# Kernel tuning notes

Measured on AMD Instinct MI355X. Metric: run time of the kernel, lower is better.

The kernel has to match this reference:

```python
import jax, jax.numpy as jnp
import numpy as np

N = 20000      # nodes
E = 200000     # edges
F_IN = 512     # num_features
H = 1024       # hidden (hard-coded in module)
OUT = 128      # output_size


def setup_inputs() -> dict:
    key = jax.random.key(0)
    ks = jax.random.split(key, 12)
    x = jax.random.normal(ks[0], (N, F_IN), jnp.float32)
    edge_index = jax.random.randint(ks[1], (2, E), 0, N, dtype=jnp.int32)
    edge_weight = jax.random.uniform(ks[2], (E,), jnp.float32)
    # GCNConv weights (glorot-ish) and biases
    w1 = jax.random.normal(ks[3], (F_IN, H), jnp.float32) / np.sqrt(F_IN)
    b1 = jnp.zeros((H,), jnp.float32)
    w2 = jax.random.normal(ks[4], (H, OUT), jnp.float32) / np.sqrt(H)
    b2 = jnp.zeros((OUT,), jnp.float32)
    # residual Linear layers
    rw1 = jax.random.normal(ks[5], (F_IN, H), jnp.float32) / np.sqrt(F_IN)
    rb1 = jax.random.normal(ks[6], (H,), jnp.float32) * 0.01
    rw2 = jax.random.normal(ks[7], (H, OUT), jnp.float32) / np.sqrt(H)
    rb2 = jax.random.normal(ks[8], (OUT,), jnp.float32) * 0.01
    return {"x": x, "w1": w1, "b1": b1, "w2": w2, "b2": b2,
            "rw1": rw1, "rb1": rb1, "rw2": rw2, "rb2": rb2,
            "edge_weight": edge_weight, "edge_index": edge_index}


def gcn_conv(x, W, b, edge_index, edge_weight, n):
    """PyG GCNConv: linear transform, add self-loops (weight 1), sym-normalized scatter-add."""
    xw = x @ W                                             # [n, d_out]
    loop = jnp.arange(n, dtype=edge_index.dtype)
    row = jnp.concatenate([edge_index[0], loop])           # sources (x_j)
    col = jnp.concatenate([edge_index[1], loop])           # targets (aggregate here)
    ew = jnp.concatenate([edge_weight, jnp.ones((n,), xw.dtype)])
    deg = jax.ops.segment_sum(ew, col, num_segments=n)     # weighted in-degree
    dis = jnp.where(deg > 0, jax.lax.rsqrt(jnp.where(deg > 0, deg, 1.0)), 0.0)
    norm = dis[row] * ew * dis[col]                        # [E+n]
    msg = xw[row] * norm[:, None]                          # gather + scale
    out = jax.ops.segment_sum(msg, col, num_segments=n)    # scatter-add
    return out + b


def reference(x, w1, b1, w2, b2, rw1, rb1, rw2, rb2, edge_weight, edge_index):
    n = x.shape[0]
    h = jax.nn.relu(gcn_conv(x, w1, b1, edge_index, edge_weight, n) + (x @ rw1 + rb1))
    # F.dropout(training=False) is identity in eval mode
    out = gcn_conv(h, w2, b2, edge_index, edge_weight, n) + (h @ rw2 + rb2)
    return out
```

## Files before the change

### kernel.cpp

```cpp
#include <hip/hip_runtime.h>
#include <hip/hip_bf16.h>

#define NN 20000
#define EE 200000
#define FIN 512
#define HID 1024
#define OUTF 128
#define MPAD 20096

typedef unsigned short ush;
typedef __attribute__((ext_vector_type(8))) short bf16x8;
typedef __attribute__((ext_vector_type(4))) float f32x4;

__device__ __forceinline__ ush f2bf_rne(float f) {
    union { float f; unsigned u; } a; a.f = f;
    unsigned u = a.u;
    return (ush)((u + 0x7fffu + ((u >> 16) & 1u)) >> 16);
}
__device__ __forceinline__ float bf2f(ush h) {
    union { float f; unsigned u; } a; a.u = ((unsigned)h) << 16;
    return a.f;
}
__device__ __forceinline__ void split_bf(float v, ush& hi, ush& lo) {
    hi = f2bf_rne(v);
    lo = f2bf_rne(v - bf2f(hi));
}

__device__ __forceinline__ void gl16(const void* g, void* l) {
    __builtin_amdgcn_global_load_lds(
        (const __attribute__((address_space(1))) unsigned*)g,
        (__attribute__((address_space(3))) unsigned*)l, 16, 0, 0);
}

__global__ void init_kernel(float* deg, int* cnt, int n) {
    int i = blockIdx.x * blockDim.x + threadIdx.x;
    if (i < n) { deg[i] = 1.0f; cnt[i] = 0; }
}

__global__ void deg_count_kernel(const int* __restrict__ ei, const float* __restrict__ ew,
                                 float* deg, int* cnt, int e) {
    int idx = blockIdx.x * blockDim.x + threadIdx.x;
    if (idx < e) {
        int c = ei[EE + idx];
        atomicAdd(&deg[c], ew[idx]);
        atomicAdd(&cnt[c], 1);
    }
}

__global__ void dis_kernel(const float* __restrict__ deg, float* dis, int n) {
    int i = blockIdx.x * blockDim.x + threadIdx.x;
    if (i < n) dis[i] = rsqrtf(deg[i]);
}

__global__ void bias_kernel(const float* __restrict__ b1, const float* __restrict__ rb1,
                            const float* __restrict__ b2, const float* __restrict__ rb2,
                            float* bias1s, float* bias2c) {
    int i = blockIdx.x * blockDim.x + threadIdx.x;
    if (i < HID) bias1s[i] = b1[i] + rb1[i];
    if (i < 256) bias2c[i] = (i < 128) ? 0.0f : (b2[i - 128] + rb2[i - 128]);
}

#define SCAN_THREADS 1024
#define SCAN_CHUNK 20
__global__ __launch_bounds__(SCAN_THREADS)
void scan_kernel(const int* __restrict__ cnt, int* rowptr, int* cursor, int n, int total_e) {
    __shared__ int part[SCAN_THREADS];
    int t = threadIdx.x;
    int base = t * SCAN_CHUNK;
    int s = 0;
    for (int j = 0; j < SCAN_CHUNK; ++j) { int i = base + j; if (i < n) s += cnt[i]; }
    part[t] = s;
    __syncthreads();
    for (int off = 1; off < SCAN_THREADS; off <<= 1) {
        int add = (t >= off) ? part[t - off] : 0;
        __syncthreads();
        part[t] += add;
        __syncthreads();
    }
    int run = (t == 0) ? 0 : part[t - 1];
    for (int j = 0; j < SCAN_CHUNK; ++j) {
        int i = base + j;
        if (i < n) { rowptr[i] = run; cursor[i] = run; run += cnt[i]; }
    }
    if (t == SCAN_THREADS - 1) rowptr[n] = total_e;
}

__global__ void scatter_kernel(const int* __restrict__ ei, const float* __restrict__ ew,
                               const float* __restrict__ dis, int* cursor,
                               int* srcs, float* norms, int e) {
    int idx = blockIdx.x * blockDim.x + threadIdx.x;
    if (idx < e) {
        int r = ei[idx];
        int c = ei[EE + idx];
        float nv = dis[r] * ew[idx] * dis[c];
        int p = atomicAdd(&cursor[c], 1);
        srcs[p] = r;
        norms[p] = nv;
    }
}

__global__ __launch_bounds__(256)
void tsplit_kernel(const float* __restrict__ src, int K, int N,
                   ush* __restrict__ dh, ush* __restrict__ dl, int ldst, int koff) {
    __shared__ float tile[32][33];
    int tx = threadIdx.x & 31, ty = threadIdx.x >> 5;
    int n0 = blockIdx.x * 32, k0 = blockIdx.y * 32;
#pragma unroll
    for (int i = 0; i < 4; ++i)
        tile[ty * 4 + i][tx] = src[(size_t)(k0 + ty * 4 + i) * N + n0 + tx];
    __syncthreads();
#pragma unroll
    for (int i = 0; i < 4; ++i) {
        int n = n0 + ty * 4 + i, k = k0 + tx;
        float v = tile[tx][ty * 4 + i];
        ush h, lo; split_bf(v, h, lo);
        size_t off = (size_t)n * ldst + koff + k;
        dh[off] = h;
        dl[off] = lo;
    }
}

__global__ __launch_bounds__(128)
void aggx_kernel(const float* __restrict__ x,
                 ush* __restrict__ xh, ush* __restrict__ xl,
                 ush* __restrict__ axh, ush* __restrict__ axl,
                 const float* __restrict__ dis,
                 const int* __restrict__ rowptr, const int* __restrict__ srcs,
                 const float* __restrict__ norms) {
    int i = blockIdx.x;
    int t = threadIdx.x;
    float d = dis[i];
    float d2 = d * d;
    float4 v = ((const float4*)(x + (size_t)i * FIN))[t];

    ushort4 vh, vl;
    split_bf(v.x, vh.x, vl.x); split_bf(v.y, vh.y, vl.y);
    split_bf(v.z, vh.z, vl.z); split_bf(v.w, vh.w, vl.w);
    ((ushort4*)(xh + (size_t)i * FIN))[t] = vh;
    ((ushort4*)(xl + (size_t)i * FIN))[t] = vl;

    float s0 = d2 * v.x, s1 = d2 * v.y, s2 = d2 * v.z, s3 = d2 * v.w;
    int beg = rowptr[i], end = rowptr[i + 1];
    int j = beg;
    for (; j + 2 <= end; j += 2) {
        int sa = srcs[j], sb = srcs[j + 1];
        float wa = norms[j], wb = norms[j + 1];
        float4 ua = ((const float4*)(x + (size_t)sa * FIN))[t];
        float4 ub = ((const float4*)(x + (size_t)sb * FIN))[t];
        s0 += wa * ua.x + wb * ub.x;
        s1 += wa * ua.y + wb * ub.y;
        s2 += wa * ua.z + wb * ub.z;
        s3 += wa * ua.w + wb * ub.w;
    }
    if (j < end) {
        int sa = srcs[j];
        float wa = norms[j];
        float4 ua = ((const float4*)(x + (size_t)sa * FIN))[t];
        s0 += wa * ua.x; s1 += wa * ua.y; s2 += wa * ua.z; s3 += wa * ua.w;
    }
    ushort4 hv, lv;
    split_bf(s0, hv.x, lv.x); split_bf(s1, hv.y, lv.y);
    split_bf(s2, hv.z, lv.z); split_bf(s3, hv.w, lv.w);
    ((ushort4*)(axh + (size_t)i * FIN))[t] = hv;
    ((ushort4*)(axl + (size_t)i * FIN))[t] = lv;
}

__global__ __launch_bounds__(256)
void gemm_mfma(const ush* __restrict__ A0h, const ush* __restrict__ A0l,
               const ush* __restrict__ A1h, const ush* __restrict__ A1l,
               int ksw, int KA,
               const ush* __restrict__ BTh, const ush* __restrict__ BTl,
               const float* __restrict__ bias,
               float* __restrict__ Cf, ush* __restrict__ Chh, ush* __restrict__ Chl,
               int M, int N, int K, int mode) {
    __shared__ ush Ah[128 * 32], Al[128 * 32], Bh[128 * 32], Bl[128 * 32];

    int t = threadIdx.x;
    int l = t & 63, w = t >> 6;
    int wr = w >> 1, wc = w & 1;
    int bm = blockIdx.y * 128, bn = blockIdx.x * 128;

    int sr = t >> 2;
    int sg8 = (t & 3) * 8;
    size_t a_off0 = (size_t)(bm + sr) * KA + sg8;
    size_t a_off1 = (size_t)(bm + 64 + sr) * KA + sg8;
    size_t b_off0 = (size_t)(bn + sr) * K + sg8;
    size_t b_off1 = (size_t)(bn + 64 + sr) * K + sg8;
    int lo0 = t * 16, lo1 = t * 16 + 4096;

    int abase = (wr * 64 + (l & 15)) * 64 + ((l >> 4) << 4);
    int bbase = (wc * 64 + (l & 15)) * 64 + ((l >> 4) << 4);

    f32x4 acc[4][4];
#pragma unroll
    for (int i = 0; i < 4; ++i)
#pragma unroll
        for (int j = 0; j < 4; ++j) acc[i][j] = (f32x4){0.f, 0.f, 0.f, 0.f};

    for (int kt = 0; kt < K; kt += 32) {
        const ush* Asrch; const ush* Asrcl; int kk;
        if (kt < ksw) { Asrch = A0h; Asrcl = A0l; kk = kt; }
        else          { Asrch = A1h; Asrcl = A1l; kk = kt - ksw; }

        gl16(Asrch + a_off0 + kk, (char*)Ah + lo0);
        gl16(Asrch + a_off1 + kk, (char*)Ah + lo1);
        gl16(Asrcl + a_off0 + kk, (char*)Al + lo0);
        gl16(Asrcl + a_off1 + kk, (char*)Al + lo1);
        gl16(BTh + b_off0 + kt, (char*)Bh + lo0);
        gl16(BTh + b_off1 + kt, (char*)Bh + lo1);
        gl16(BTl + b_off0 + kt, (char*)Bl + lo0);
        gl16(BTl + b_off1 + kt, (char*)Bl + lo1);
        __syncthreads();

        bf16x8 ah[4], al[4], bh[4], bl[4];
#pragma unroll
        for (int f = 0; f < 4; ++f) {
            ah[f] = *(const bf16x8*)((const char*)Ah + abase + f * 1024);
            al[f] = *(const bf16x8*)((const char*)Al + abase + f * 1024);
            bh[f] = *(const bf16x8*)((const char*)Bh + bbase + f * 1024);
            bl[f] = *(const bf16x8*)((const char*)Bl + bbase + f * 1024);
        }
#pragma unroll
        for (int fm = 0; fm < 4; ++fm)
#pragma unroll
            for (int fn = 0; fn < 4; ++fn)
                acc[fm][fn] = __builtin_amdgcn_mfma_f32_16x16x32_bf16(ah[fm], bh[fn], acc[fm][fn], 0, 0, 0);
#pragma unroll
        for (int fm = 0; fm < 4; ++fm)
#pragma unroll
            for (int fn = 0; fn < 4; ++fn)
                acc[fm][fn] = __builtin_amdgcn_mfma_f32_16x16x32_bf16(ah[fm], bl[fn], acc[fm][fn], 0, 0, 0);
#pragma unroll
        for (int fm = 0; fm < 4; ++fm)
#pragma unroll
            for (int fn = 0; fn < 4; ++fn)
                acc[fm][fn] = __builtin_amdgcn_mfma_f32_16x16x32_bf16(al[fm], bh[fn], acc[fm][fn], 0, 0, 0);
        __syncthreads();
    }

    int ccol = bn + wc * 64 + (l & 15);
    float bb[4];
#pragma unroll
    for (int fn = 0; fn < 4; ++fn) bb[fn] = bias ? bias[ccol + fn * 16] : 0.0f;

    if (mode) {
#pragma unroll
        for (int fm = 0; fm < 4; ++fm)
#pragma unroll
            for (int j = 0; j < 4; ++j) {
                int row = bm + wr * 64 + fm * 16 + ((l >> 4) << 2) + j;
                if (row < M) {
#pragma unroll
                    for (int fn = 0; fn < 4; ++fn) {
                        float v = fmaxf(acc[fm][fn][j] + bb[fn], 0.0f);
                        ush hi, lo; split_bf(v, hi, lo);
                        size_t off = (size_t)row * N + ccol + fn * 16;
                        Chh[off] = hi;
                        Chl[off] = lo;
                    }
                }
            }
    } else {
#pragma unroll
        for (int fm = 0; fm < 4; ++fm)
#pragma unroll
            for (int j = 0; j < 4; ++j) {
                int row = bm + wr * 64 + fm * 16 + ((l >> 4) << 2) + j;
                if (row < M) {
#pragma unroll
                    for (int fn = 0; fn < 4; ++fn)
                        Cf[(size_t)row * N + ccol + fn * 16] = acc[fm][fn][j] + bb[fn];
                }
            }
    }
}

__global__ __launch_bounds__(256)
void agg2_kernel(const float* __restrict__ z2, const float* __restrict__ dis,
                 const int* __restrict__ rowptr, const int* __restrict__ srcs,
                 const float* __restrict__ norms, float* __restrict__ out) {
    int wave = threadIdx.x >> 6;
    int lane = threadIdx.x & 63;
    int i = blockIdx.x * 4 + wave;
    float d = dis[i];
    float d2 = d * d;
    float2 v = ((const float2*)(z2 + (size_t)i * 256))[lane];
    float ax = d2 * v.x, ay = d2 * v.y;
    int beg = rowptr[i], end = rowptr[i + 1];
    int j = beg;
    for (; j + 2 <= end; j += 2) {
        int sa = srcs[j], sb = srcs[j + 1];
        float wa = norms[j], wb = norms[j + 1];
        float2 ua = ((const float2*)(z2 + (size_t)sa * 256))[lane];
        float2 ub = ((const float2*)(z2 + (size_t)sb * 256))[lane];
        ax += wa * ua.x + wb * ub.x;
        ay += wa * ua.y + wb * ub.y;
    }
    if (j < end) {
        int sa = srcs[j];
        float wa = norms[j];
        float2 ua = ((const float2*)(z2 + (size_t)sa * 256))[lane];
        ax += wa * ua.x; ay += wa * ua.y;
    }
    float2 r = ((const float2*)(z2 + (size_t)i * 256 + 128))[lane];
    float2 o; o.x = ax + r.x; o.y = ay + r.y;
    ((float2*)(out + (size_t)i * OUTF))[lane] = o;
}

extern "C" void kernel_launch(void* const* d_in, const int* in_sizes, int n_in,
                              void* d_out, int out_size, void* d_ws, size_t ws_size,
                              hipStream_t stream) {
    const float* x   = (const float*)d_in[0];
    const float* w1  = (const float*)d_in[1];
    const float* b1  = (const float*)d_in[2];
    const float* w2  = (const float*)d_in[3];
    const float* b2  = (const float*)d_in[4];
    const float* rw1 = (const float*)d_in[5];
    const float* rb1 = (const float*)d_in[6];
    const float* rw2 = (const float*)d_in[7];
    const float* rb2 = (const float*)d_in[8];
    const float* ew  = (const float*)d_in[9];
    const int*   ei  = (const int*)d_in[10];
    float* out = (float*)d_out;

    char* p = (char*)d_ws;
    ush* xh  = (ush*)p; p += (size_t)MPAD * FIN * 2;
    ush* xl  = (ush*)p; p += (size_t)MPAD * FIN * 2;
    ush* axh = (ush*)p; p += (size_t)MPAD * FIN * 2;
    ush* axl = (ush*)p; p += (size_t)MPAD * FIN * 2;
    ush* hh  = (ush*)p; p += (size_t)MPAD * HID * 2;
    ush* hl  = (ush*)p; p += (size_t)MPAD * HID * 2;
    ush* w1cth = (ush*)p; p += (size_t)HID * HID * 2;
    ush* w1ctl = (ush*)p; p += (size_t)HID * HID * 2;
    ush* w2cth = (ush*)p; p += (size_t)256 * HID * 2;
    ush* w2ctl = (ush*)p; p += (size_t)256 * HID * 2;
    float* deg    = (float*)p; p += NN * 4;
    float* dis    = (float*)p; p += NN * 4;
    float* norms  = (float*)p; p += EE * 4;
    float* bias1s = (float*)p; p += HID * 4;
    float* bias2c = (float*)p; p += 256 * 4;
    int* rowptr = (int*)p; p += (NN + 1) * 4;
    int* cursor = (int*)p; p += NN * 4;
    int* cnt    = (int*)p; p += NN * 4;
    int* srcs   = (int*)p; p += EE * 4;
    float* z2 = (float*)xh;

    init_kernel<<<(NN + 255) / 256, 256, 0, stream>>>(deg, cnt, NN);
    deg_count_kernel<<<(EE + 255) / 256, 256, 0, stream>>>(ei, ew, deg, cnt, EE);
    dis_kernel<<<(NN + 255) / 256, 256, 0, stream>>>(deg, dis, NN);
    bias_kernel<<<(HID + 255) / 256, 256, 0, stream>>>(b1, rb1, b2, rb2, bias1s, bias2c);
    scan_kernel<<<1, SCAN_THREADS, 0, stream>>>(cnt, rowptr, cursor, NN, EE);
    scatter_kernel<<<(EE + 255) / 256, 256, 0, stream>>>(ei, ew, dis, cursor, srcs, norms, EE);

    { dim3 g(HID / 32, FIN / 32); tsplit_kernel<<<g, 256, 0, stream>>>(w1,  FIN, HID, w1cth, w1ctl, HID, 0);   }
    { dim3 g(HID / 32, FIN / 32); tsplit_kernel<<<g, 256, 0, stream>>>(rw1, FIN, HID, w1cth, w1ctl, HID, FIN); }
    { dim3 g(OUTF / 32, HID / 32); tsplit_kernel<<<g, 256, 0, stream>>>(w2,  HID, OUTF, w2cth, w2ctl, HID, 0); }
    { dim3 g(OUTF / 32, HID / 32); tsplit_kernel<<<g, 256, 0, stream>>>(rw2, HID, OUTF,
                                        w2cth + (size_t)128 * HID, w2ctl + (size_t)128 * HID, HID, 0); }

    aggx_kernel<<<NN, 128, 0, stream>>>(x, xh, xl, axh, axl, dis, rowptr, srcs, norms);

    {
        dim3 grid(HID / 128, MPAD / 128);
        gemm_mfma<<<grid, 256, 0, stream>>>(axh, axl, xh, xl, FIN, FIN,
                                            w1cth, w1ctl, bias1s,
                                            nullptr, hh, hl,
                                            NN, HID, HID, 1);
    }
    {
        dim3 grid(256 / 128, MPAD / 128);
        gemm_mfma<<<grid, 256, 0, stream>>>(hh, hl, hh, hl, HID, HID,
                                            w2cth, w2ctl, bias2c,
                                            z2, nullptr, nullptr,
                                            NN, 256, HID, 0);
    }
    agg2_kernel<<<NN / 4, 256, 0, stream>>>(z2, dis, rowptr, srcs, norms, out);
}
```

Before: 467.9 us.

## Double-buffer LDS tiles in MFMA GEMM and remap workgroups across XCDs

```diff
diff --git a/kernel.cpp b/kernel.cpp
--- a/kernel.cpp
+++ b/kernel.cpp
@@ -173,12 +173,19 @@
                const float* __restrict__ bias,
                float* __restrict__ Cf, ush* __restrict__ Chh, ush* __restrict__ Chl,
                int M, int N, int K, int mode) {
-    __shared__ ush Ah[128 * 32], Al[128 * 32], Bh[128 * 32], Bl[128 * 32];
+    __shared__ ush Ah[2][128 * 32], Al[2][128 * 32], Bh[2][128 * 32], Bl[2][128 * 32];
+
+    int nwg = gridDim.x * gridDim.y;
+    int orig = blockIdx.y * gridDim.x + blockIdx.x;
+    int xcd = orig & 7, slot = orig >> 3;
+    int q = nwg >> 3, r = nwg & 7;
+    int wg = (xcd < r ? xcd * (q + 1) : r * (q + 1) + (xcd - r) * q) + slot;
+    int bn = (wg % gridDim.x) * 128;
+    int bm = (wg / gridDim.x) * 128;
 
     int t = threadIdx.x;
     int l = t & 63, w = t >> 6;
     int wr = w >> 1, wc = w & 1;
-    int bm = blockIdx.y * 128, bn = blockIdx.x * 128;
 
     int sr = t >> 2;
     int sg8 = (t & 3) * 8;
@@ -191,34 +198,40 @@
     int abase = (wr * 64 + (l & 15)) * 64 + ((l >> 4) << 4);
     int bbase = (wc * 64 + (l & 15)) * 64 + ((l >> 4) << 4);
 
-    f32x4 acc[4][4];
-#pragma unroll
-    for (int i = 0; i < 4; ++i)
-#pragma unroll
-        for (int j = 0; j < 4; ++j) acc[i][j] = (f32x4){0.f, 0.f, 0.f, 0.f};
-
-    for (int kt = 0; kt < K; kt += 32) {
+    auto stage = [&](int kt, int b) {
         const ush* Asrch; const ush* Asrcl; int kk;
         if (kt < ksw) { Asrch = A0h; Asrcl = A0l; kk = kt; }
         else          { Asrch = A1h; Asrcl = A1l; kk = kt - ksw; }
-
-        gl16(Asrch + a_off0 + kk, (char*)Ah + lo0);
-        gl16(Asrch + a_off1 + kk, (char*)Ah + lo1);
-        gl16(Asrcl + a_off0 + kk, (char*)Al + lo0);
-        gl16(Asrcl + a_off1 + kk, (char*)Al + lo1);
-        gl16(BTh + b_off0 + kt, (char*)Bh + lo0);
-        gl16(BTh + b_off1 + kt, (char*)Bh + lo1);
-        gl16(BTl + b_off0 + kt, (char*)Bl + lo0);
-        gl16(BTl + b_off1 + kt, (char*)Bl + lo1);
-        __syncthreads();
+        gl16(Asrch + a_off0 + kk, (char*)Ah[b] + lo0);
+        gl16(Asrch + a_off1 + kk, (char*)Ah[b] + lo1);
+        gl16(Asrcl + a_off0 + kk, (char*)Al[b] + lo0);
+        gl16(Asrcl + a_off1 + kk, (char*)Al[b] + lo1);
+        gl16(BTh + b_off0 + kt, (char*)Bh[b] + lo0);
+        gl16(BTh + b_off1 + kt, (char*)Bh[b] + lo1);
+        gl16(BTl + b_off0 + kt, (char*)Bl[b] + lo0);
+        gl16(BTl + b_off1 + kt, (char*)Bl[b] + lo1);
+    };
+
+    f32x4 acc[4][4];
+#pragma unroll
+    for (int i = 0; i < 4; ++i)
+#pragma unroll
+        for (int j = 0; j < 4; ++j) acc[i][j] = (f32x4){0.f, 0.f, 0.f, 0.f};
+
+    stage(0, 0);
+    __syncthreads();
+
+    int cur = 0;
+    for (int kt = 0; kt < K; kt += 32) {
+        if (kt + 32 < K) stage(kt + 32, cur ^ 1);
 
         bf16x8 ah[4], al[4], bh[4], bl[4];
 #pragma unroll
         for (int f = 0; f < 4; ++f) {
-            ah[f] = *(const bf16x8*)((const char*)Ah + abase + f * 1024);
-            al[f] = *(const bf16x8*)((const char*)Al + abase + f * 1024);
-            bh[f] = *(const bf16x8*)((const char*)Bh + bbase + f * 1024);
-            bl[f] = *(const bf16x8*)((const char*)Bl + bbase + f * 1024);
+            ah[f] = *(const bf16x8*)((const char*)Ah[cur] + abase + f * 1024);
+            al[f] = *(const bf16x8*)((const char*)Al[cur] + abase + f * 1024);
+            bh[f] = *(const bf16x8*)((const char*)Bh[cur] + bbase + f * 1024);
+            bl[f] = *(const bf16x8*)((const char*)Bl[cur] + bbase + f * 1024);
         }
 #pragma unroll
         for (int fm = 0; fm < 4; ++fm)
@@ -235,7 +248,9 @@
 #pragma unroll
             for (int fn = 0; fn < 4; ++fn)
                 acc[fm][fn] = __builtin_amdgcn_mfma_f32_16x16x32_bf16(al[fm], bh[fn], acc[fm][fn], 0, 0, 0);
+
         __syncthreads();
+        cur ^= 1;
     }
 
     int ccol = bn + wc * 64 + (l & 15);
```

New measurement: 465.2 us. No clear change (-0.6%).

## Remap GEMM workgroups per XCD and fold small setup kernels together

Applied to the files above, without the earlier changes.

```diff
diff --git a/kernel.cpp b/kernel.cpp
--- a/kernel.cpp
+++ b/kernel.cpp
@@ -6,7 +6,7 @@
 #define FIN 512
 #define HID 1024
 #define OUTF 128
-#define MPAD 20096
+#define MPAD 20224
 
 typedef unsigned short ush;
 typedef __attribute__((ext_vector_type(8))) short bf16x8;
@@ -32,9 +32,14 @@
         (__attribute__((address_space(3))) unsigned*)l, 16, 0, 0);
 }
 
-__global__ void init_kernel(float* deg, int* cnt, int n) {
+__global__ void init_kernel(float* deg, int* cnt, int n,
+                            const float* __restrict__ b1, const float* __restrict__ rb1,
+                            const float* __restrict__ b2, const float* __restrict__ rb2,
+                            float* bias1s, float* bias2c) {
     int i = blockIdx.x * blockDim.x + threadIdx.x;
     if (i < n) { deg[i] = 1.0f; cnt[i] = 0; }
+    if (i < HID) bias1s[i] = b1[i] + rb1[i];
+    if (i < 256) bias2c[i] = (i < 128) ? 0.0f : (b2[i - 128] + rb2[i - 128]);
 }
 
 __global__ void deg_count_kernel(const int* __restrict__ ei, const float* __restrict__ ew,
@@ -47,28 +52,19 @@
     }
 }
 
-__global__ void dis_kernel(const float* __restrict__ deg, float* dis, int n) {
-    int i = blockIdx.x * blockDim.x + threadIdx.x;
-    if (i < n) dis[i] = rsqrtf(deg[i]);
-}
-
-__global__ void bias_kernel(const float* __restrict__ b1, const float* __restrict__ rb1,
-                            const float* __restrict__ b2, const float* __restrict__ rb2,
-                            float* bias1s, float* bias2c) {
-    int i = blockIdx.x * blockDim.x + threadIdx.x;
-    if (i < HID) bias1s[i] = b1[i] + rb1[i];
-    if (i < 256) bias2c[i] = (i < 128) ? 0.0f : (b2[i - 128] + rb2[i - 128]);
-}
-
 #define SCAN_THREADS 1024
 #define SCAN_CHUNK 20
 __global__ __launch_bounds__(SCAN_THREADS)
-void scan_kernel(const int* __restrict__ cnt, int* rowptr, int* cursor, int n, int total_e) {
+void scan_kernel(const int* __restrict__ cnt, int* rowptr, int* cursor, int n, int total_e,
+                 const float* __restrict__ deg, float* __restrict__ dis) {
     __shared__ int part[SCAN_THREADS];
     int t = threadIdx.x;
     int base = t * SCAN_CHUNK;
     int s = 0;
-    for (int j = 0; j < SCAN_CHUNK; ++j) { int i = base + j; if (i < n) s += cnt[i]; }
+    for (int j = 0; j < SCAN_CHUNK; ++j) {
+        int i = base + j;
+        if (i < n) { s += cnt[i]; dis[i] = rsqrtf(deg[i]); }
+    }
     part[t] = s;
     __syncthreads();
     for (int off = 1; off < SCAN_THREADS; off <<= 1) {
@@ -175,10 +171,17 @@
                int M, int N, int K, int mode) {
     __shared__ ush Ah[128 * 32], Al[128 * 32], Bh[128 * 32], Bl[128 * 32];
 
+    int nwg = gridDim.x * gridDim.y;
+    int orig = blockIdx.y * gridDim.x + blockIdx.x;
+    int xcd = orig & 7, slot = orig >> 3;
+    int q = nwg >> 3, r = nwg & 7;
+    int wg = (xcd < r ? xcd * (q + 1) : r * (q + 1) + (xcd - r) * q) + slot;
+    int bn = (wg % gridDim.x) * 128;
+    int bm = (wg / gridDim.x) * 128;
+
     int t = threadIdx.x;
     int l = t & 63, w = t >> 6;
     int wr = w >> 1, wc = w & 1;
-    int bm = blockIdx.y * 128, bn = blockIdx.x * 128;
 
     int sr = t >> 2;
     int sg8 = (t & 3) * 8;
@@ -302,8 +305,8 @@
         float2 ua = ((const float2*)(z2 + (size_t)sa * 256))[lane];
         ax += wa * ua.x; ay += wa * ua.y;
     }
-    float2 r = ((const float2*)(z2 + (size_t)i * 256 + 128))[lane];
-    float2 o; o.x = ax + r.x; o.y = ay + r.y;
+    float2 rr = ((const float2*)(z2 + (size_t)i * 256 + 128))[lane];
+    float2 o; o.x = ax + rr.x; o.y = ay + rr.y;
     ((float2*)(out + (size_t)i * OUTF))[lane] = o;
 }
 
@@ -345,11 +348,9 @@
     int* srcs   = (int*)p; p += EE * 4;
     float* z2 = (float*)xh;
 
-    init_kernel<<<(NN + 255) / 256, 256, 0, stream>>>(deg, cnt, NN);
+    init_kernel<<<(NN + 255) / 256, 256, 0, stream>>>(deg, cnt, NN, b1, rb1, b2, rb2, bias1s, bias2c);
     deg_count_kernel<<<(EE + 255) / 256, 256, 0, stream>>>(ei, ew, deg, cnt, EE);
-    dis_kernel<<<(NN + 255) / 256, 256, 0, stream>>>(deg, dis, NN);
-    bias_kernel<<<(HID + 255) / 256, 256, 0, stream>>>(b1, rb1, b2, rb2, bias1s, bias2c);
-    scan_kernel<<<1, SCAN_THREADS, 0, stream>>>(cnt, rowptr, cursor, NN, EE);
+    scan_kernel<<<1, SCAN_THREADS, 0, stream>>>(cnt, rowptr, cursor, NN, EE, deg, dis);
     scatter_kernel<<<(EE + 255) / 256, 256, 0, stream>>>(ei, ew, dis, cursor, srcs, norms, EE);
 
     { dim3 g(HID / 32, FIN / 32); tsplit_kernel<<<g, 256, 0, stream>>>(w1,  FIN, HID, w1cth, w1ctl, HID, 0);   }
```

After: 463.2 us. Within noise of the previous version (-1.0%).
